# Kernel optimization log

Measured on AMD Instinct MI355X. Metric: run time of the kernel, lower is better.

## Reference

```python
import jax, jax.numpy as jnp
import numpy as np

N_ENTITIES = 100000
EMBED = 64
BATCH = 4096
TEMPERATURE = 0.2


def _infonce(v1, v2, temperature):
    # v1, v2: [B, d]
    B = v1.shape[0]
    sim11 = v1 @ v1.T  # [B,B]
    sim22 = v2 @ v2.T
    sim12 = v1 @ v2.T
    eye = jnp.eye(B, dtype=bool)
    neg_inf = jnp.float32(-jnp.inf)
    sim11 = jnp.where(eye, neg_inf, sim11)
    sim22 = jnp.where(eye, neg_inf, sim22)
    logits1 = jnp.concatenate([sim12, sim11], axis=-1)          # [B,2B]
    logits2 = jnp.concatenate([sim22, sim12.T], axis=-1)        # [B,2B]
    logits = jnp.concatenate([logits1, logits2], axis=0) / temperature  # [2B,2B]
    targets = jnp.arange(2 * B)
    logp = jax.nn.log_softmax(logits, axis=-1)
    return -jnp.mean(jnp.take_along_axis(logp, targets[:, None], axis=-1))


def setup_inputs() -> dict:
    key = jax.random.key(0)
    k1, k2, k3, k4, k5, k6 = jax.random.split(key, 6)
    return {
        "input_u_list": jax.random.randint(k1, (BATCH,), 0, N_ENTITIES),
        "input_i_list": jax.random.randint(k2, (BATCH,), 0, N_ENTITIES),
        "u_sub1_embeddings": jax.random.normal(k3, (N_ENTITIES, EMBED), dtype=jnp.float32),
        "i_sub1_embeddings": jax.random.normal(k4, (N_ENTITIES, EMBED), dtype=jnp.float32),
        "u_sub2_embeddings": jax.random.normal(k5, (N_ENTITIES, EMBED), dtype=jnp.float32),
        "i_sub2_embeddings": jax.random.normal(k6, (N_ENTITIES, EMBED), dtype=jnp.float32),
    }


def reference(input_u_list, input_i_list, u_sub1_embeddings, i_sub1_embeddings,
              u_sub2_embeddings, i_sub2_embeddings):
    # user branch: gather + L2-normalize
    u1 = u_sub1_embeddings[input_u_list]
    u2 = u_sub2_embeddings[input_u_list]
    u1 = u1 / jnp.linalg.norm(u1, axis=1, keepdims=True)
    u2 = u2 / jnp.linalg.norm(u2, axis=1, keepdims=True)
    user_cl_loss = _infonce(u1, u2, TEMPERATURE)
    # item branch: gather only (the original does NOT normalize items)
    i1 = i_sub1_embeddings[input_i_list]
    i2 = i_sub2_embeddings[input_i_list]
    item_cl_loss = _infonce(i1, i2, TEMPERATURE)
    return user_cl_loss + item_cl_loss
```

## Files before the change

kernel.cpp:

```cpp
#include <hip/hip_runtime.h>
#include <hip/hip_bf16.h>
#include <math.h>

#define B_SZ   4096
#define D      64
#define RPB    8192
#define NCHUNK 8
#define TPC    8
#define NPART  16
#define LN2    0.69314718055994531f
#define PRESCALE 2.6857914f

typedef __attribute__((ext_vector_type(8))) short  bf16x8;
typedef __attribute__((ext_vector_type(4))) float  f32x4;

__device__ __forceinline__ float fexp2(float x) { return __builtin_amdgcn_exp2f(x); }


__global__ __launch_bounds__(256) void gather_kernel(
    const int* __restrict__ u_idx, const int* __restrict__ i_idx,
    const float* __restrict__ u1e, const float* __restrict__ i1e,
    const float* __restrict__ u2e, const float* __restrict__ i2e,
    __hip_bfloat16* __restrict__ Xbf, float* __restrict__ dots)
{
    const int tid  = threadIdx.x;
    const int wave = tid >> 6, lane = tid & 63;
    const int g      = blockIdx.x * 4 + wave;
    const int branch = g >> 12;
    const int i      = g & (B_SZ - 1);
    const int idx    = (branch == 0) ? u_idx[i] : i_idx[i];
    const float* s1  = (branch == 0) ? u1e : i1e;
    const float* s2  = (branch == 0) ? u2e : i2e;

    float v1 = s1[(size_t)idx * D + lane];
    float v2 = s2[(size_t)idx * D + lane];
    if (branch == 0) {
        float a = v1 * v1, b = v2 * v2;
        #pragma unroll
        for (int o = 32; o > 0; o >>= 1) {
            a += __shfl_xor(a, o, 64);
            b += __shfl_xor(b, o, 64);
        }
        v1 *= rsqrtf(a);
        v2 *= rsqrtf(b);
    }
    float p = v1 * v2;
    #pragma unroll
    for (int o = 32; o > 0; o >>= 1) p += __shfl_xor(p, o, 64);
    if (lane == 0) dots[g] = p;

    const size_t row1 = (size_t)branch * RPB + i;
    Xbf[row1 * D + lane]          = __float2bfloat16(v1 * PRESCALE);
    Xbf[(row1 + B_SZ) * D + lane] = __float2bfloat16(v2 * PRESCALE);
}

template<int IS_USER>
__global__ __launch_bounds__(256, 3) void gram_lse_kernel(
    const __hip_bfloat16* __restrict__ Xb, float2* __restrict__ P)
{
    __shared__ __align__(16) __hip_bfloat16 Bs[128][72];

    const int tid   = threadIdx.x;
    const int bx    = blockIdx.x;
    const int chunk = blockIdx.y;
    const int r0    = bx * 128;

    const int wave = tid >> 6, lane = tid & 63;
    const int wm = wave >> 1, wn = wave & 1;
    const int quad = lane >> 4, tx = lane & 15;

    #pragma unroll
    for (int p = 0; p < 4; ++p) {
        int e = p * 256 + tid;
        int row = e >> 3, c8 = e & 7;
        *(uint4*)&Bs[row][c8 * 8] =
            *(const uint4*)(Xb + (size_t)(r0 + row) * D + c8 * 8);
    }
    __syncthreads();
    bf16x8 afr[4][2];
    #pragma unroll
    for (int mt = 0; mt < 4; ++mt)
        #pragma unroll
        for (int ks = 0; ks < 2; ++ks)
            afr[mt][ks] = *(const bf16x8*)&Bs[wm * 64 + mt * 16 + tx][ks * 32 + quad * 8];

    float m_run[16], s_run[16];
    #pragma unroll
    for (int r = 0; r < 16; ++r) { m_run[r] = -INFINITY; s_run[r] = 0.f; }

    const int lrq  = wm * 64 + quad * 4;
    const int lcol = wn * 64 + tx;

    for (int t = 0; t < TPC; ++t) {
        const int ct = chunk * TPC + t;
        const int c0 = ct * 128;
        __syncthreads();
        #pragma unroll
        for (int p = 0; p < 4; ++p) {
            int e = p * 256 + tid;
            int row = e >> 3, c8 = e & 7;
            *(uint4*)&Bs[row][c8 * 8] =
                *(const uint4*)(Xb + (size_t)(c0 + row) * D + c8 * 8);
        }
        __syncthreads();

        f32x4 acc[4][4];
        const f32x4 z = {0.f, 0.f, 0.f, 0.f};
        #pragma unroll
        for (int nt = 0; nt < 4; ++nt) {
            const bf16x8 b0 = *(const bf16x8*)&Bs[wn * 64 + nt * 16 + tx][quad * 8];
            #pragma unroll
            for (int mt = 0; mt < 4; ++mt)
                acc[mt][nt] = __builtin_amdgcn_mfma_f32_16x16x32_bf16(afr[mt][0], b0, z, 0, 0, 0);
        }
        #pragma unroll
        for (int nt = 0; nt < 4; ++nt) {
            const bf16x8 b1 = *(const bf16x8*)&Bs[wn * 64 + nt * 16 + tx][32 + quad * 8];
            #pragma unroll
            for (int mt = 0; mt < 4; ++mt)
                acc[mt][nt] = __builtin_amdgcn_mfma_f32_16x16x32_bf16(afr[mt][1], b1, acc[mt][nt], 0, 0, 0);
        }

        const bool diag = (ct == bx);
        #pragma unroll
        for (int mt = 0; mt < 4; ++mt) {
            #pragma unroll
            for (int rr = 0; rr < 4; ++rr) {
                float y0 = acc[mt][0][rr], y1 = acc[mt][1][rr],
                      y2 = acc[mt][2][rr], y3 = acc[mt][3][rr];
                if (diag) {
                    const int dr = lrq + mt * 16 + rr - lcol;
                    if (dr == 0)  y0 = -INFINITY;
                    if (dr == 16) y1 = -INFINITY;
                    if (dr == 32) y2 = -INFINITY;
                    if (dr == 48) y3 = -INFINITY;
                }
                const int r = mt * 4 + rr;
                if (IS_USER) {
                    s_run[r] += fexp2(y0) + fexp2(y1) + fexp2(y2) + fexp2(y3);
                } else {
                    float mx   = fmaxf(fmaxf(y0, y1), fmaxf(y2, y3));
                    float newm = fmaxf(m_run[r], mx);
                    s_run[r] = s_run[r] * fexp2(m_run[r] - newm)
                             + fexp2(y0 - newm) + fexp2(y1 - newm)
                             + fexp2(y2 - newm) + fexp2(y3 - newm);
                    m_run[r] = newm;
                }
            }
        }
    }

    #pragma unroll
    for (int r = 0; r < 16; ++r) {
        float m = IS_USER ? 0.f : m_run[r];
        float s = s_run[r];
        #pragma unroll
        for (int o = 1; o < 16; o <<= 1) {
            if (IS_USER) {
                s += __shfl_xor(s, o, 64);
            } else {
                float om = __shfl_xor(m, o, 64);
                float os = __shfl_xor(s, o, 64);
                float M  = fmaxf(m, om);
                s = s * fexp2(m - M) + os * fexp2(om - M);
                m = M;
            }
        }
        if (tx == 0) {
            const int grow = r0 + wm * 64 + (r >> 2) * 16 + quad * 4 + (r & 3);
            P[(size_t)grow * NPART + chunk * 2 + wn] = make_float2(m, s);
        }
    }
}

__global__ __launch_bounds__(256) void merge_kernel(
    const float2* __restrict__ P, const float* __restrict__ dots,
    float* __restrict__ out)
{
    __shared__ float red[4];
    const int tid  = threadIdx.x;
    const int wave = tid >> 6, lane = tid & 63;
    const int gw   = blockIdx.x * 4 + wave;
    const int row  = gw * 4 + (lane >> 4);
    const int c    = lane & 15;

    float2 p = P[(size_t)row * NPART + c];
    float m = p.x, s = p.y;
    #pragma unroll
    for (int o = 1; o < 16; o <<= 1) {
        float om = __shfl_xor(m, o, 64);
        float os = __shfl_xor(s, o, 64);
        float M  = fmaxf(m, om);
        s = s * fexp2(m - M) + os * fexp2(om - M);
        m = M;
    }

    float v = 0.f;
    if ((lane & 15) == 0)
        v = LN2 * (m + log2f(s)) * (1.0f / (float)RPB);
    if (tid < 8)
        v -= dots[blockIdx.x * 8 + tid] * (5.0f / (float)B_SZ);

    #pragma unroll
    for (int o = 32; o > 0; o >>= 1) v += __shfl_xor(v, o, 64);
    if (lane == 0) red[wave] = v;
    __syncthreads();
    if (tid == 0)
        atomicAdd(out, red[0] + red[1] + red[2] + red[3]);
}

extern "C" void kernel_launch(void* const* d_in, const int* in_sizes, int n_in,
                              void* d_out, int out_size, void* d_ws, size_t ws_size,
                              hipStream_t stream) {
    const int*   u_idx = (const int*)d_in[0];
    const int*   i_idx = (const int*)d_in[1];
    const float* u1e   = (const float*)d_in[2];
    const float* i1e   = (const float*)d_in[3];
    const float* u2e   = (const float*)d_in[4];
    const float* i2e   = (const float*)d_in[5];
    float* out = (float*)d_out;

    __hip_bfloat16* Xbf = (__hip_bfloat16*)d_ws;
    float*  dots = (float*)((char*)d_ws + 2 * RPB * D * 2);
    float2* P    = (float2*)((char*)dots + RPB * sizeof(float));

    hipMemsetAsync(out, 0, sizeof(float), stream);

    gather_kernel<<<dim3(2048), dim3(256), 0, stream>>>(
        u_idx, i_idx, u1e, i1e, u2e, i2e, Xbf, dots);
    gram_lse_kernel<1><<<dim3(64, NCHUNK), dim3(256), 0, stream>>>(Xbf, P);
    gram_lse_kernel<0><<<dim3(64, NCHUNK), dim3(256), 0, stream>>>(
        Xbf + (size_t)RPB * D, P + (size_t)RPB * NPART);
    merge_kernel<<<dim3(1024), dim3(256), 0, stream>>>(P, dots, out);
}
```

Measured before the change: 176.0 us.

## Drop LDS staging in gram kernel, fuse branches into one launch, shrink merge grid

The gram kernel now loads A and B MFMA fragments straight from global memory into registers, with no LDS staging and no __syncthreads. The user and item branches are merged into one launch via blockIdx.z, so 1024 blocks fill the GPU together. The merge kernel has each block handle 8 virtual blocks, cutting its block count and atomics eightfold. Direct global loads rely on L1/L2 hits and may raise memory latency and register pressure, while the larger grid removes one launch and its tail.

```diff
diff --git a/kernel.cpp b/kernel.cpp
--- a/kernel.cpp
+++ b/kernel.cpp
@@ -55,11 +55,9 @@
 }
 
 template<int IS_USER>
-__global__ __launch_bounds__(256, 3) void gram_lse_kernel(
+__device__ __forceinline__ void gram_body(
     const __hip_bfloat16* __restrict__ Xb, float2* __restrict__ P)
 {
-    __shared__ __align__(16) __hip_bfloat16 Bs[128][72];
-
     const int tid   = threadIdx.x;
     const int bx    = blockIdx.x;
     const int chunk = blockIdx.y;
@@ -69,20 +67,13 @@
     const int wm = wave >> 1, wn = wave & 1;
     const int quad = lane >> 4, tx = lane & 15;
 
-    #pragma unroll
-    for (int p = 0; p < 4; ++p) {
-        int e = p * 256 + tid;
-        int row = e >> 3, c8 = e & 7;
-        *(uint4*)&Bs[row][c8 * 8] =
-            *(const uint4*)(Xb + (size_t)(r0 + row) * D + c8 * 8);
-    }
-    __syncthreads();
     bf16x8 afr[4][2];
+    const __hip_bfloat16* Ap = Xb + (size_t)(r0 + wm * 64 + tx) * D + quad * 8;
     #pragma unroll
     for (int mt = 0; mt < 4; ++mt)
         #pragma unroll
         for (int ks = 0; ks < 2; ++ks)
-            afr[mt][ks] = *(const bf16x8*)&Bs[wm * 64 + mt * 16 + tx][ks * 32 + quad * 8];
+            afr[mt][ks] = *(const bf16x8*)(Ap + mt * 16 * D + ks * 32);
 
     float m_run[16], s_run[16];
     #pragma unroll
@@ -91,35 +82,32 @@
     const int lrq  = wm * 64 + quad * 4;
     const int lcol = wn * 64 + tx;
 
+    const __hip_bfloat16* Bbase =
+        Xb + (size_t)(chunk * TPC * 128 + wn * 64 + tx) * D + quad * 8;
+
     for (int t = 0; t < TPC; ++t) {
         const int ct = chunk * TPC + t;
-        const int c0 = ct * 128;
-        __syncthreads();
-        #pragma unroll
-        for (int p = 0; p < 4; ++p) {
-            int e = p * 256 + tid;
-            int row = e >> 3, c8 = e & 7;
-            *(uint4*)&Bs[row][c8 * 8] =
-                *(const uint4*)(Xb + (size_t)(c0 + row) * D + c8 * 8);
-        }
-        __syncthreads();
+        const __hip_bfloat16* Bp = Bbase + (size_t)t * 128 * D;
+
+        bf16x8 b0[4], b1[4];
+        #pragma unroll
+        for (int nt = 0; nt < 4; ++nt) {
+            b0[nt] = *(const bf16x8*)(Bp + nt * 16 * D);
+            b1[nt] = *(const bf16x8*)(Bp + nt * 16 * D + 32);
+        }
 
         f32x4 acc[4][4];
         const f32x4 z = {0.f, 0.f, 0.f, 0.f};
         #pragma unroll
-        for (int nt = 0; nt < 4; ++nt) {
-            const bf16x8 b0 = *(const bf16x8*)&Bs[wn * 64 + nt * 16 + tx][quad * 8];
+        for (int nt = 0; nt < 4; ++nt)
             #pragma unroll
             for (int mt = 0; mt < 4; ++mt)
-                acc[mt][nt] = __builtin_amdgcn_mfma_f32_16x16x32_bf16(afr[mt][0], b0, z, 0, 0, 0);
-        }
-        #pragma unroll
-        for (int nt = 0; nt < 4; ++nt) {
-            const bf16x8 b1 = *(const bf16x8*)&Bs[wn * 64 + nt * 16 + tx][32 + quad * 8];
+                acc[mt][nt] = __builtin_amdgcn_mfma_f32_16x16x32_bf16(afr[mt][0], b0[nt], z, 0, 0, 0);
+        #pragma unroll
+        for (int nt = 0; nt < 4; ++nt)
             #pragma unroll
             for (int mt = 0; mt < 4; ++mt)
-                acc[mt][nt] = __builtin_amdgcn_mfma_f32_16x16x32_bf16(afr[mt][1], b1, acc[mt][nt], 0, 0, 0);
-        }
+                acc[mt][nt] = __builtin_amdgcn_mfma_f32_16x16x32_bf16(afr[mt][1], b1[nt], acc[mt][nt], 0, 0, 0);
 
         const bool diag = (ct == bx);
         #pragma unroll
@@ -173,6 +161,16 @@
     }
 }
 
+__global__ __launch_bounds__(256, 3) void gram_lse_fused(
+    const __hip_bfloat16* __restrict__ Xb0, float2* __restrict__ P0)
+{
+    const int branch = blockIdx.z;
+    const __hip_bfloat16* Xb = Xb0 + (size_t)branch * RPB * D;
+    float2* P = P0 + (size_t)branch * RPB * NPART;
+    if (branch == 0) gram_body<1>(Xb, P);
+    else             gram_body<0>(Xb, P);
+}
+
 __global__ __launch_bounds__(256) void merge_kernel(
     const float2* __restrict__ P, const float* __restrict__ dots,
     float* __restrict__ out)
@@ -180,27 +178,33 @@
     __shared__ float red[4];
     const int tid  = threadIdx.x;
     const int wave = tid >> 6, lane = tid & 63;
-    const int gw   = blockIdx.x * 4 + wave;
-    const int row  = gw * 4 + (lane >> 4);
-    const int c    = lane & 15;
-
-    float2 p = P[(size_t)row * NPART + c];
-    float m = p.x, s = p.y;
-    #pragma unroll
-    for (int o = 1; o < 16; o <<= 1) {
-        float om = __shfl_xor(m, o, 64);
-        float os = __shfl_xor(s, o, 64);
-        float M  = fmaxf(m, om);
-        s = s * fexp2(m - M) + os * fexp2(om - M);
-        m = M;
-    }
-
-    float v = 0.f;
-    if ((lane & 15) == 0)
-        v = LN2 * (m + log2f(s)) * (1.0f / (float)RPB);
-    if (tid < 8)
-        v -= dots[blockIdx.x * 8 + tid] * (5.0f / (float)B_SZ);
-
+
+    float vsum = 0.f;
+    #pragma unroll
+    for (int k = 0; k < 8; ++k) {
+        const int vb  = blockIdx.x * 8 + k;
+        const int gw  = vb * 4 + wave;
+        const int row = gw * 4 + (lane >> 4);
+        const int c   = lane & 15;
+
+        float2 p = P[(size_t)row * NPART + c];
+        float m = p.x, s = p.y;
+        #pragma unroll
+        for (int o = 1; o < 16; o <<= 1) {
+            float om = __shfl_xor(m, o, 64);
+            float os = __shfl_xor(s, o, 64);
+            float M  = fmaxf(m, om);
+            s = s * fexp2(m - M) + os * fexp2(om - M);
+            m = M;
+        }
+
+        if ((lane & 15) == 0)
+            vsum += LN2 * (m + log2f(s)) * (1.0f / (float)RPB);
+        if (tid < 8)
+            vsum -= dots[vb * 8 + tid] * (5.0f / (float)B_SZ);
+    }
+
+    float v = vsum;
     #pragma unroll
     for (int o = 32; o > 0; o >>= 1) v += __shfl_xor(v, o, 64);
     if (lane == 0) red[wave] = v;
@@ -228,8 +232,6 @@
 
     gather_kernel<<<dim3(2048), dim3(256), 0, stream>>>(
         u_idx, i_idx, u1e, i1e, u2e, i2e, Xbf, dots);
-    gram_lse_kernel<1><<<dim3(64, NCHUNK), dim3(256), 0, stream>>>(Xbf, P);
-    gram_lse_kernel<0><<<dim3(64, NCHUNK), dim3(256), 0, stream>>>(
-        Xbf + (size_t)RPB * D, P + (size_t)RPB * NPART);
-    merge_kernel<<<dim3(1024), dim3(256), 0, stream>>>(P, dots, out);
-}
+    gram_lse_fused<<<dim3(64, NCHUNK, 2), dim3(256), 0, stream>>>(Xbf, P);
+    merge_kernel<<<dim3(128), dim3(256), 0, stream>>>(P, dots, out);
+}
```

Result: no change. 173.3 us (-1.6%).
